# Kernel tuning notes

Measured on AMD Instinct MI355X. Metric: run time of the kernel, lower is better.

The kernel has to match this reference:

```python
import jax, jax.numpy as jnp
import numpy as np

N_NODES = 100000


def setup_inputs() -> dict:
    key = jax.random.key(0)
    k1, k2, k3 = jax.random.split(key, 3)
    emb = jax.random.normal(k1, (N_NODES, 64), dtype=jnp.float32)
    src = jax.random.randint(k2, (1250000,), 0, N_NODES, dtype=jnp.int64)
    dst = jax.random.randint(k3, (1250000,), 0, N_NODES, dtype=jnp.int64)
    return {"emb": emb, "src": src, "dst": dst}


def reference(emb, src, dst):
    # DGL GraphConv(norm='both', weight=False, bias=False):
    #   out = D_in^{-1/2} * A * (D_out^{-1/2} * emb), degrees clamped to >= 1.
    n = emb.shape[0]
    e = src.shape[0]
    ones = jnp.ones((e,), dtype=emb.dtype)
    out_deg = jax.ops.segment_sum(ones, src, num_segments=n)  # out-degree of src nodes
    in_deg = jax.ops.segment_sum(ones, dst, num_segments=n)   # in-degree of dst nodes
    src_norm = jnp.clip(out_deg, 1.0, None) ** -0.5           # [N]
    dst_norm = jnp.clip(in_deg, 1.0, None) ** -0.5            # [N]
    h = emb * src_norm[:, None]                               # [N, D] pre-normalize
    msg = h[src]                                              # [E, D] gather
    agg = jax.ops.segment_sum(msg, dst, num_segments=n)       # [N, D] scatter-add
    return agg * dst_norm[:, None]
```

## Files before the change

kernel.cpp:

```cpp
#include <hip/hip_runtime.h>
#include <hip/hip_fp16.h>

#define NNODES 100000
#define DIM 64
#define TILE 256
#define NTILES ((NNODES + TILE - 1) / TILE)
#define NTPAD 392
#define CAP 4096
#define EPT 16
#define BIN_THREADS 512
#define BIN_CHUNK (BIN_THREADS * EPT)

__global__ void convert_kernel(const float* __restrict__ emb, const float* __restrict__ src_norm,
                               __half* __restrict__ embh, int total8) {
    int i = blockIdx.x * blockDim.x + threadIdx.x;
    if (i < total8) {
        int base = i * 8;
        float w = src_norm[base >> 6];
        float4 a = *(const float4*)(emb + base);
        float4 b = *(const float4*)(emb + base + 4);
        __half2* o = (__half2*)(embh + base);
        o[0] = __floats2half2_rn(a.x * w, a.y * w);
        o[1] = __floats2half2_rn(a.z * w, a.w * w);
        o[2] = __floats2half2_rn(b.x * w, b.y * w);
        o[3] = __floats2half2_rn(b.z * w, b.w * w);
    }
}

__global__ __launch_bounds__(BIN_THREADS) void bin_kernel(
        const int* __restrict__ src, const int* __restrict__ dst,
        int* __restrict__ gcurD, int* __restrict__ gcurS,
        unsigned int* __restrict__ binnedD, int* __restrict__ binnedS, int E) {
    __shared__ int histD[NTPAD], histS[NTPAD], baseD[NTPAD], baseS[NTPAD];
    __shared__ unsigned short rankD[BIN_CHUNK], rankS[BIN_CHUNK];
    int tid = threadIdx.x;
    for (int t = tid; t < NTPAD; t += BIN_THREADS) { histD[t] = 0; histS[t] = 0; }
    __syncthreads();
    int base = blockIdx.x * BIN_CHUNK;
    #pragma unroll
    for (int i = 0; i < EPT; i++) {
        int idx = base + i * BIN_THREADS + tid;
        if (idx < E) {
            int d = dst[idx];
            int s = src[idx];
            rankD[i * BIN_THREADS + tid] = (unsigned short)atomicAdd(&histD[d >> 8], 1);
            rankS[i * BIN_THREADS + tid] = (unsigned short)atomicAdd(&histS[s >> 8], 1);
        }
    }
    __syncthreads();
    for (int t = tid; t < NTPAD; t += BIN_THREADS) {
        int h = histD[t];
        baseD[t] = h ? atomicAdd(&gcurD[t], h) : 0;
        h = histS[t];
        baseS[t] = h ? atomicAdd(&gcurS[t], h) : 0;
    }
    __syncthreads();
    #pragma unroll
    for (int i = 0; i < EPT; i++) {
        int idx = base + i * BIN_THREADS + tid;
        if (idx < E) {
            int d = dst[idx];
            int s = src[idx];
            int tD = d >> 8, tS = s >> 8;
            int pD = baseD[tD] + (int)rankD[i * BIN_THREADS + tid];
            int pS = baseS[tS] + (int)rankS[i * BIN_THREADS + tid];
            if (pD < CAP) binnedD[(size_t)tD * CAP + pD] = ((unsigned)(d & 255) << 17) | (unsigned)s;
            if (pS < CAP) binnedS[(size_t)tS * CAP + pS] = s;
        }
    }
}

__global__ __launch_bounds__(256) void sortnorm_kernel(
        const int* __restrict__ gcurS, const int* __restrict__ binnedS,
        const int* __restrict__ gcurD, const unsigned int* __restrict__ binnedD,
        float* __restrict__ src_norm, int* __restrict__ sortedD,
        int* __restrict__ offs, int* __restrict__ deg) {
    __shared__ int cnt[TILE];
    __shared__ int cur[TILE];
    __shared__ int wsum[4];
    __shared__ int tot_s;
    int t = blockIdx.x, tid = threadIdx.x;
    int node = t * TILE + tid;
    cnt[tid] = 0;
    __syncthreads();
    {
        int lenS = min(gcurS[t], CAP);
        const int* segS = binnedS + (size_t)t * CAP;
        for (int j = tid; j < lenS; j += 256)
            atomicAdd(&cnt[segS[j] & 255], 1);
    }
    __syncthreads();
    if (node < NNODES)
        src_norm[node] = rsqrtf(fmaxf((float)cnt[tid], 1.0f));
    __syncthreads();
    cnt[tid] = 0;
    __syncthreads();
    int len = min(gcurD[t], CAP);
    const unsigned int* seg = binnedD + (size_t)t * CAP;
    for (int j = tid; j < len; j += 256)
        atomicAdd(&cnt[seg[j] >> 17], 1);
    __syncthreads();
    int v = cnt[tid];
    int vpad = (v + 3) & ~3;
    int lane = tid & 63, w = tid >> 6;
    int x = vpad;
    #pragma unroll
    for (int off = 1; off < 64; off <<= 1) {
        int y = __shfl_up(x, off, 64);
        if (lane >= off) x += y;
    }
    if (lane == 63) wsum[w] = x;
    __syncthreads();
    int add = 0;
    #pragma unroll
    for (int k = 0; k < 4; k++) add += (k < w) ? wsum[k] : 0;
    int ex = x - vpad + add;
    cur[tid] = ex;
    if (tid == 255) tot_s = ex + vpad;
    __syncthreads();
    for (int j = tid; j < len; j += 256) {
        unsigned int p = seg[j];
        int dl = p >> 17;
        int pos = atomicAdd(&cur[dl], 1);
        if (pos < CAP) sortedD[(size_t)t * CAP + pos] = (int)(p & 0x1FFFF);
    }
    __syncthreads();
    int pe = ex + vpad;
    for (int p = cur[tid]; p < pe && p < CAP; p++) sortedD[(size_t)t * CAP + p] = 0;
    for (int k = tot_s + tid; k < CAP; k += 256) sortedD[(size_t)t * CAP + k] = 0;
    if (node < NNODES) {
        offs[node] = t * CAP + ex;
        deg[node] = v;
    }
}

__global__ __launch_bounds__(256) void agg3_kernel(
        const __half* __restrict__ embh, const int* __restrict__ offs,
        const int* __restrict__ deg, const int* __restrict__ sortedD,
        float* __restrict__ out, int n) {
    int wid = threadIdx.x >> 6;
    int lane = threadIdx.x & 63;
    int node = blockIdx.x * 4 + wid;
    if (node >= n) return;
    int m = deg[node];
    const int* run = sortedD + offs[node];
    int hs = lane >> 5;
    int fp = lane & 31;
    float accx = 0.0f, accy = 0.0f;
    for (int j = 0; j < m; j += 8) {
        int4 a = *(const int4*)(run + j);
        int4 b = *(const int4*)(run + j + 4);
        int s0 = hs ? a.y : a.x;
        int s1 = hs ? a.w : a.z;
        int s2 = hs ? b.y : b.x;
        int s3 = hs ? b.w : b.z;
        __half2 h0 = *(const __half2*)(embh + ((size_t)s0 << 6) + fp * 2);
        __half2 h1 = *(const __half2*)(embh + ((size_t)s1 << 6) + fp * 2);
        __half2 h2 = *(const __half2*)(embh + ((size_t)s2 << 6) + fp * 2);
        __half2 h3 = *(const __half2*)(embh + ((size_t)s3 << 6) + fp * 2);
        float m0 = (j + 0 + hs < m) ? 1.0f : 0.0f;
        float m1 = (j + 2 + hs < m) ? 1.0f : 0.0f;
        float m2 = (j + 4 + hs < m) ? 1.0f : 0.0f;
        float m3 = (j + 6 + hs < m) ? 1.0f : 0.0f;
        float2 f0 = __half22float2(h0);
        float2 f1 = __half22float2(h1);
        float2 f2 = __half22float2(h2);
        float2 f3 = __half22float2(h3);
        accx = fmaf(f0.x, m0, accx); accy = fmaf(f0.y, m0, accy);
        accx = fmaf(f1.x, m1, accx); accy = fmaf(f1.y, m1, accy);
        accx = fmaf(f2.x, m2, accx); accy = fmaf(f2.y, m2, accy);
        accx = fmaf(f3.x, m3, accx); accy = fmaf(f3.y, m3, accy);
    }
    float dn = rsqrtf(fmaxf((float)m, 1.0f));
    float sx = (accx + __shfl_xor(accx, 32)) * dn;
    float sy = (accy + __shfl_xor(accy, 32)) * dn;
    if (lane < 32) {
        float2 o = make_float2(sx, sy);
        *(float2*)(out + ((size_t)node << 6) + fp * 2) = o;
    }
}

extern "C" void kernel_launch(void* const* d_in, const int* in_sizes, int n_in,
                              void* d_out, int out_size, void* d_ws, size_t ws_size,
                              hipStream_t stream) {
    const float* emb = (const float*)d_in[0];
    const int* src = (const int*)d_in[1];
    const int* dst = (const int*)d_in[2];
    int E = in_sizes[1];
    float* out = (float*)d_out;

    int* gcurD = (int*)d_ws;
    int* gcurS = gcurD + NTPAD;
    unsigned int* binnedD = (unsigned int*)(gcurS + NTPAD);
    int* binnedS = (int*)(binnedD + (size_t)NTILES * CAP);
    int* sortedD = binnedS;
    int* offs = binnedS + (size_t)NTILES * CAP;
    int* deg = offs + NNODES;
    float* src_norm = (float*)(deg + NNODES);
    __half* embh = (__half*)(src_norm + NNODES);

    hipMemsetAsync(gcurD, 0, 2 * NTPAD * sizeof(int), stream);

    int bin_blocks = (E + BIN_CHUNK - 1) / BIN_CHUNK;
    bin_kernel<<<bin_blocks, BIN_THREADS, 0, stream>>>(src, dst, gcurD, gcurS, binnedD, binnedS, E);

    sortnorm_kernel<<<NTILES, 256, 0, stream>>>(gcurS, binnedS, gcurD, binnedD,
                                                src_norm, sortedD, offs, deg);

    int total8 = NNODES * DIM / 8;
    convert_kernel<<<(total8 + 255) / 256, 256, 0, stream>>>(emb, src_norm, embh, total8);

    agg3_kernel<<<(NNODES + 3) / 4, 256, 0, stream>>>(embh, offs, deg, sortedD, out, NNODES);
}
```

Baseline: 104.3 us.

## Gather 16-byte neighbor rows with 8 lanes per edge and sentinel zero row

The aggregation kernel now assigns 8 lanes to each neighbor, and each lane loads 16 bytes (8 halves) of the row. A wavefront therefore processes 8 neighbors per iteration with wide loads instead of 4-byte loads, and the partial sums are combined with an xor-shuffle tree. Runs are padded to multiples of 8 and filled with a sentinel index that points to a zero row appended after the half-precision embeddings, which removes the per-edge masking. CAP grows to absorb the extra padding, which enlarges the workspace and adds more wasted gathers from the zero row.

```diff
diff --git a/kernel.cpp b/kernel.cpp
--- a/kernel.cpp
+++ b/kernel.cpp
@@ -6,7 +6,7 @@
 #define TILE 256
 #define NTILES ((NNODES + TILE - 1) / TILE)
 #define NTPAD 392
-#define CAP 4096
+#define CAP 4608
 #define EPT 16
 #define BIN_THREADS 512
 #define BIN_CHUNK (BIN_THREADS * EPT)
@@ -24,6 +24,11 @@
         o[1] = __floats2half2_rn(a.z * w, a.w * w);
         o[2] = __floats2half2_rn(b.x * w, b.y * w);
         o[3] = __floats2half2_rn(b.z * w, b.w * w);
+    } else if (i - total8 < 8) {
+        int k = i - total8;
+        __half2* o = (__half2*)(embh + (size_t)NNODES * DIM + k * 8);
+        __half2 z = __floats2half2_rn(0.0f, 0.0f);
+        o[0] = z; o[1] = z; o[2] = z; o[3] = z;
     }
 }
 
@@ -101,7 +106,7 @@
         atomicAdd(&cnt[seg[j] >> 17], 1);
     __syncthreads();
     int v = cnt[tid];
-    int vpad = (v + 3) & ~3;
+    int vpad = (v + 7) & ~7;
     int lane = tid & 63, w = tid >> 6;
     int x = vpad;
     #pragma unroll
@@ -126,15 +131,15 @@
     }
     __syncthreads();
     int pe = ex + vpad;
-    for (int p = cur[tid]; p < pe && p < CAP; p++) sortedD[(size_t)t * CAP + p] = 0;
-    for (int k = tot_s + tid; k < CAP; k += 256) sortedD[(size_t)t * CAP + k] = 0;
+    for (int p = cur[tid]; p < pe && p < CAP; p++) sortedD[(size_t)t * CAP + p] = NNODES;
+    for (int k = tot_s + tid; k < CAP; k += 256) sortedD[(size_t)t * CAP + k] = NNODES;
     if (node < NNODES) {
         offs[node] = t * CAP + ex;
         deg[node] = v;
     }
 }
 
-__global__ __launch_bounds__(256) void agg3_kernel(
+__global__ __launch_bounds__(256) void agg4_kernel(
         const __half* __restrict__ embh, const int* __restrict__ offs,
         const int* __restrict__ deg, const int* __restrict__ sortedD,
         float* __restrict__ out, int n) {
@@ -144,39 +149,39 @@
     if (node >= n) return;
     int m = deg[node];
     const int* run = sortedD + offs[node];
-    int hs = lane >> 5;
-    int fp = lane & 31;
-    float accx = 0.0f, accy = 0.0f;
+    int slot = lane >> 3;
+    int oct = lane & 7;
+    float a0 = 0.f, a1 = 0.f, a2 = 0.f, a3 = 0.f, a4 = 0.f, a5 = 0.f, a6 = 0.f, a7 = 0.f;
     for (int j = 0; j < m; j += 8) {
-        int4 a = *(const int4*)(run + j);
-        int4 b = *(const int4*)(run + j + 4);
-        int s0 = hs ? a.y : a.x;
-        int s1 = hs ? a.w : a.z;
-        int s2 = hs ? b.y : b.x;
-        int s3 = hs ? b.w : b.z;
-        __half2 h0 = *(const __half2*)(embh + ((size_t)s0 << 6) + fp * 2);
-        __half2 h1 = *(const __half2*)(embh + ((size_t)s1 << 6) + fp * 2);
-        __half2 h2 = *(const __half2*)(embh + ((size_t)s2 << 6) + fp * 2);
-        __half2 h3 = *(const __half2*)(embh + ((size_t)s3 << 6) + fp * 2);
-        float m0 = (j + 0 + hs < m) ? 1.0f : 0.0f;
-        float m1 = (j + 2 + hs < m) ? 1.0f : 0.0f;
-        float m2 = (j + 4 + hs < m) ? 1.0f : 0.0f;
-        float m3 = (j + 6 + hs < m) ? 1.0f : 0.0f;
-        float2 f0 = __half22float2(h0);
-        float2 f1 = __half22float2(h1);
-        float2 f2 = __half22float2(h2);
-        float2 f3 = __half22float2(h3);
-        accx = fmaf(f0.x, m0, accx); accy = fmaf(f0.y, m0, accy);
-        accx = fmaf(f1.x, m1, accx); accy = fmaf(f1.y, m1, accy);
-        accx = fmaf(f2.x, m2, accx); accy = fmaf(f2.y, m2, accy);
-        accx = fmaf(f3.x, m3, accx); accy = fmaf(f3.y, m3, accy);
+        int idx = run[j + slot];
+        float4 hv = *(const float4*)(embh + ((size_t)idx << 6) + (oct << 3));
+        const __half2* hp = (const __half2*)&hv;
+        float2 f0 = __half22float2(hp[0]);
+        float2 f1 = __half22float2(hp[1]);
+        float2 f2 = __half22float2(hp[2]);
+        float2 f3 = __half22float2(hp[3]);
+        a0 += f0.x; a1 += f0.y;
+        a2 += f1.x; a3 += f1.y;
+        a4 += f2.x; a5 += f2.y;
+        a6 += f3.x; a7 += f3.y;
+    }
+    #pragma unroll
+    for (int off = 8; off < 64; off <<= 1) {
+        a0 += __shfl_xor(a0, off);
+        a1 += __shfl_xor(a1, off);
+        a2 += __shfl_xor(a2, off);
+        a3 += __shfl_xor(a3, off);
+        a4 += __shfl_xor(a4, off);
+        a5 += __shfl_xor(a5, off);
+        a6 += __shfl_xor(a6, off);
+        a7 += __shfl_xor(a7, off);
     }
     float dn = rsqrtf(fmaxf((float)m, 1.0f));
-    float sx = (accx + __shfl_xor(accx, 32)) * dn;
-    float sy = (accy + __shfl_xor(accy, 32)) * dn;
-    if (lane < 32) {
-        float2 o = make_float2(sx, sy);
-        *(float2*)(out + ((size_t)node << 6) + fp * 2) = o;
+    if (lane < 16) {
+        int half = lane >> 3;
+        float4 o = half ? make_float4(a4 * dn, a5 * dn, a6 * dn, a7 * dn)
+                        : make_float4(a0 * dn, a1 * dn, a2 * dn, a3 * dn);
+        *(float4*)(out + ((size_t)node << 6) + (oct << 3) + (half << 2)) = o;
     }
 }
 
@@ -208,7 +213,7 @@
                                                 src_norm, sortedD, offs, deg);
 
     int total8 = NNODES * DIM / 8;
-    convert_kernel<<<(total8 + 255) / 256, 256, 0, stream>>>(emb, src_norm, embh, total8);
-
-    agg3_kernel<<<(NNODES + 3) / 4, 256, 0, stream>>>(embh, offs, deg, sortedD, out, NNODES);
-}
+    convert_kernel<<<(total8 + 8 + 255) / 256, 256, 0, stream>>>(emb, src_norm, embh, total8);
+
+    agg4_kernel<<<(NNODES + 3) / 4, 256, 0, stream>>>(embh, offs, deg, sortedD, out, NNODES);
+}
```

New measurement: 105.4 us. About the same (+1.0%).
